# Optimization experiments

Measured on AMD Instinct MI355X. Metric: run time of the kernel, lower is better.

The kernel has to match this reference:

```python
import jax, jax.numpy as jnp
import numpy as np

B, D, E, K = 32768, 512, 64, 4
NCTX = 16
H = (NCTX // 2 - 1) * 768  # 5376: per-expert context block, (n_ctx/2 - 1) rows of ctx_dim=768
NOISE_EPS = 1e-2
LOSS_COEF = 1e-2


def setup_inputs() -> dict:
    key = jax.random.key(0)
    ks = jax.random.split(key, 5)
    x = jax.random.normal(ks[0], (B, D), jnp.float32)
    w_gate = jax.random.normal(ks[1], (D, E), jnp.float32) * 0.02
    w_noise = jax.random.normal(ks[2], (D, E), jnp.float32) * 0.02
    noise = jax.random.normal(ks[3], (B, E), jnp.float32)
    ctx_c = jax.random.normal(ks[4], (E, H), jnp.float32) * 0.02
    return {"x": x, "w_gate": w_gate, "w_noise": w_noise, "noise": noise, "ctx_c": ctx_c}


def _cv_squared(v, eps=1e-10):
    # coefficient-of-variation squared: var / mean^2
    return jnp.var(v) / (jnp.mean(v) ** 2 + eps)


def _normal_cdf(z):
    return 0.5 * (1.0 + jax.lax.erf(z * (1.0 / np.sqrt(2.0))))


def reference(x, w_gate, w_noise, noise, ctx_c):
    # ---- noisy top-k gating (Shazeer sparsely-gated MoE) ----
    clean_logits = x @ w_gate                                    # [B, E]
    noise_stddev = jax.nn.softplus(x @ w_noise) + NOISE_EPS      # [B, E]
    noisy_logits = clean_logits + noise * noise_stddev           # [B, E]

    top_logits, top_idx = jax.lax.top_k(noisy_logits, K + 1)     # [B, K+1]
    top_k_logits = top_logits[:, :K]
    top_k_idx = top_idx[:, :K]
    top_k_gates = jax.nn.softmax(top_k_logits, axis=-1)          # [B, K]

    rows = jnp.arange(B)[:, None]
    gates = jnp.zeros((B, E), x.dtype).at[rows, top_k_idx].set(top_k_gates)  # sparse -> dense scatter

    # ---- load-balancing aux loss ----
    importance = gates.sum(axis=0)                               # [E]
    thr_in = top_logits[:, K][:, None]                           # (K+1)-th largest noisy logit
    thr_out = top_logits[:, K - 1][:, None]                      # K-th largest noisy logit
    is_in = noisy_logits > thr_in
    prob_in = _normal_cdf((clean_logits - thr_in) / noise_stddev)
    prob_out = _normal_cdf((clean_logits - thr_out) / noise_stddev)
    load = jnp.where(is_in, prob_in, prob_out).sum(axis=0)       # [E]
    aux_loss = (_cv_squared(importance) + _cv_squared(load)) * LOSS_COEF

    # ---- weighted combine of per-expert context vectors (as in LPromptLearner) ----
    out = jnp.einsum('be,eh->bh', gates, ctx_c)                  # [B, H]
    return out, aux_loss
```

## Files before the change

### kernel.cpp

```cpp
#include <hip/hip_runtime.h>
#include <math.h>

#define B_ 32768
#define D_ 512
#define E_ 64
#define H_ 5376
#define H4_ (H_ / 4)
#define HC_ 128
#define NCH_ (H_ / HC_)

typedef float f32x4 __attribute__((ext_vector_type(4)));
typedef _Float16 f16x8 __attribute__((ext_vector_type(8)));

__device__ __forceinline__ unsigned short f16bits(_Float16 h) {
    union { _Float16 h; unsigned short u; } c; c.h = h; return c.u;
}

__global__ __launch_bounds__(256) void prep_kernel(
    const float* __restrict__ wgate, const float* __restrict__ wnoise,
    _Float16* __restrict__ wt0, _Float16* __restrict__ wt1)
{
    int e = blockIdx.x;
    int n  = e >> 4, le = e & 15;
    const float* src = (e < E_) ? (wgate + e) : (wnoise + (e - E_));
    for (int k = threadIdx.x; k < D_; k += 256) {
        float v = src[(size_t)k * E_] * 1024.0f;
        _Float16 h0 = (_Float16)v;
        _Float16 h1 = (_Float16)(v - (float)h0);
        int ks = k >> 5, g = (k & 31) >> 3, j = k & 7;
        size_t idx = ((size_t)(ks * 8 + n) * 64 + g * 16 + le) * 8 + j;
        wt0[idx] = h0;
        wt1[idx] = h1;
    }
}

#define TOP5_STEP(TV, TI)                                              \
    {                                                                  \
        double bm = v0; int bj = 0;                                    \
        if (v1 > bm) { bm = v1; bj = 1; }                              \
        if (v2 > bm) { bm = v2; bj = 2; }                              \
        if (v3 > bm) { bm = v3; bj = 3; }                              \
        int be = bj * 16 + le;                                         \
        _Pragma("unroll")                                              \
        for (int off = 1; off < 16; off <<= 1) {                       \
            double om = __shfl_xor(bm, off, 64);                       \
            int    oe = __shfl_xor(be, off, 64);                       \
            if (om > bm || (om == bm && oe < be)) { bm = om; be = oe; }\
        }                                                              \
        TV = bm; TI = be;                                              \
        bool wn = ((be & 15) == le); int sl = be >> 4;                 \
        v0 = (wn && sl == 0) ? -1.0e300 : v0;                          \
        v1 = (wn && sl == 1) ? -1.0e300 : v1;                          \
        v2 = (wn && sl == 2) ? -1.0e300 : v2;                          \
        v3 = (wn && sl == 3) ? -1.0e300 : v3;                          \
    }

__global__ __launch_bounds__(256) void gate_kernel(
    const float* __restrict__ x,
    const _Float16* __restrict__ wt0,
    const _Float16* __restrict__ wt1,
    const float* __restrict__ noise,
    unsigned int* __restrict__ o_idx,
    float4* __restrict__ o_g,
    float* __restrict__ g_imp,
    float* __restrict__ g_load)
{
    __shared__ float s_imp[E_];
    __shared__ float s_load[E_];

    const int t  = threadIdx.x;
    const int w  = t >> 6;
    const int l  = t & 63;
    const int le = l & 15;
    const int g  = l >> 4;
    const int b0 = blockIdx.x * 64;

    if (t < E_) { s_imp[t] = 0.0f; s_load[t] = 0.0f; }
    __syncthreads();

    f32x4 accAC[8], accB[8];
#pragma unroll
    for (int n = 0; n < 8; ++n) {
        accAC[n] = (f32x4){0.f, 0.f, 0.f, 0.f};
        accB[n]  = (f32x4){0.f, 0.f, 0.f, 0.f};
    }

    const float* abase = x + (size_t)(b0 + w * 16 + le) * D_ + g * 8;

#pragma unroll 4
    for (int ks = 0; ks < 16; ++ks) {
        float4 va = *(const float4*)(abase + ks * 32);
        float4 vb = *(const float4*)(abase + ks * 32 + 4);
        float vv[8] = {va.x, va.y, va.z, va.w, vb.x, vb.y, vb.z, vb.w};
        f16x8 a0, a1;
#pragma unroll
        for (int j = 0; j < 8; ++j) {
            float vs = vv[j] * 16.0f;
            _Float16 h = (_Float16)vs;
            a0[j] = h;
            a1[j] = (_Float16)((vs - (float)h) * 4096.0f);
        }
#pragma unroll
        for (int n = 0; n < 8; ++n) {
            size_t boff = ((size_t)(ks * 8 + n) * 64 + l) * 8;
            f16x8 b0f = *(const f16x8*)(wt0 + boff);
            f16x8 b1f = *(const f16x8*)(wt1 + boff);
            accAC[n] = __builtin_amdgcn_mfma_f32_16x16x32_f16(a0, b0f, accAC[n], 0, 0, 0);
            accAC[n] = __builtin_amdgcn_mfma_f32_16x16x32_f16(a0, b1f, accAC[n], 0, 0, 0);
            accB[n]  = __builtin_amdgcn_mfma_f32_16x16x32_f16(a1, b0f, accB[n],  0, 0, 0);
        }
    }

    const double UNSCALE = 1.0 / 16384.0;
    const double RESC    = 1.0 / 4096.0;
    float loadacc[4] = {0.f, 0.f, 0.f, 0.f};
#pragma unroll
    for (int r = 0; r < 4; ++r) {
        int li = w * 16 + g * 4 + r;
        int b  = b0 + li;
        double cl[4], ny[4];
        float  sdf[4];
#pragma unroll
        for (int n = 0; n < 4; ++n) {
            cl[n] = ((double)accAC[n][r] + (double)accB[n][r] * RESC) * UNSCALE;
            float z = (float)(((double)accAC[n+4][r] + (double)accB[n+4][r] * RESC) * UNSCALE);
            float sp = (z > 20.0f) ? z : log1pf(expf(z));
            sdf[n] = sp + 0.01f;
            float nz = noise[(size_t)b * E_ + le + 16 * n];
            ny[n] = cl[n] + (double)(nz * sdf[n]);
        }
        double v0 = ny[0], v1 = ny[1], v2 = ny[2], v3 = ny[3];
        double tv0, tv1, tv2, tv3, tv4;
        int    ti0, ti1, ti2, ti3, ti4;
        TOP5_STEP(tv0, ti0)
        TOP5_STEP(tv1, ti1)
        TOP5_STEP(tv2, ti2)
        TOP5_STEP(tv3, ti3)
        TOP5_STEP(tv4, ti4)
        float e1 = expf((float)(tv1 - tv0)),
              e2 = expf((float)(tv2 - tv0)),
              e3 = expf((float)(tv3 - tv0));
        float inv = 1.0f / (1.0f + e1 + e2 + e3);
        float g0 = inv, g1 = e1 * inv, g2 = e2 * inv, g3 = e3 * inv;
        if (le == 0) {
            o_idx[b] = (unsigned)ti0 | ((unsigned)ti1 << 8) |
                       ((unsigned)ti2 << 16) | ((unsigned)ti3 << 24);
            float4 gv; gv.x = g0; gv.y = g1; gv.z = g2; gv.w = g3;
            o_g[b] = gv;
            atomicAdd(&s_imp[ti0], g0);
            atomicAdd(&s_imp[ti1], g1);
            atomicAdd(&s_imp[ti2], g2);
            atomicAdd(&s_imp[ti3], g3);
        }
        double thr_out = tv3;
        double thr_in  = tv4;
#pragma unroll
        for (int n = 0; n < 4; ++n) {
            double thr = (ny[n] > thr_in) ? thr_in : thr_out;
            float  zz  = (float)(cl[n] - thr) / sdf[n];
            loadacc[n] += 0.5f * (1.0f + erff(zz * 0.70710678118654752f));
        }
    }
#pragma unroll
    for (int n = 0; n < 4; ++n) atomicAdd(&s_load[16 * n + le], loadacc[n]);
    __syncthreads();
    if (t < E_) {
        atomicAdd(&g_imp[t],  s_imp[t]);
        atomicAdd(&g_load[t], s_load[t]);
    }
}

__global__ __launch_bounds__(256) void dispatch_kernel(
    const float* __restrict__ ctx,
    const unsigned int* __restrict__ o_idx,
    const float4* __restrict__ o_g,
    float* __restrict__ out)
{
    __shared__ f32x4 cs[E_ * (HC_ / 4)];

    const int t  = threadIdx.x;
    const int h0 = blockIdx.x * HC_;
    const int tb = blockIdx.y * 64;

#pragma unroll
    for (int i = 0; i < 8; ++i) {
        int idx = t + 256 * i;
        int e = idx >> 5, c = idx & 31;
        cs[idx] = *(const f32x4*)&ctx[(size_t)e * H_ + h0 + c * 4];
    }
    __syncthreads();

    const int tok = t >> 5;
    const int c   = t & 31;
#pragma unroll
    for (int s = 0; s < 8; ++s) {
        int b = tb + s * 8 + tok;
        unsigned pk = o_idx[b];
        float4 g = o_g[b];
        f32x4 r = g.x * cs[((pk      ) & 255u) * 32 + c]
                + g.y * cs[((pk >>  8) & 255u) * 32 + c]
                + g.z * cs[((pk >> 16) & 255u) * 32 + c]
                + g.w * cs[( pk >> 24         ) * 32 + c];
        __builtin_nontemporal_store(r, (f32x4*)&out[(size_t)b * H_ + h0 + c * 4]);
    }
}

__global__ void loss_kernel(const float* __restrict__ g_imp,
                            const float* __restrict__ g_load,
                            float* __restrict__ out)
{
    int e = threadIdx.x;
    double vi = (double)g_imp[e];
    double vl = (double)g_load[e];
    double si = vi, sl = vl;
#pragma unroll
    for (int off = 1; off < 64; off <<= 1) {
        si += __shfl_xor(si, off, 64);
        sl += __shfl_xor(sl, off, 64);
    }
    double mi = si / 64.0, ml = sl / 64.0;
    double di = vi - mi, dl = vl - ml;
    double qi = di * di, ql = dl * dl;
#pragma unroll
    for (int off = 1; off < 64; off <<= 1) {
        qi += __shfl_xor(qi, off, 64);
        ql += __shfl_xor(ql, off, 64);
    }
    double vari = qi / 64.0, varl = ql / 64.0;
    double cv2i = vari / (mi * mi + 1e-10);
    double cv2l = varl / (ml * ml + 1e-10);
    if (e == 0) out[(size_t)B_ * H_] = (float)((cv2i + cv2l) * 0.01);
}

extern "C" void kernel_launch(void* const* d_in, const int* in_sizes, int n_in,
                              void* d_out, int out_size, void* d_ws, size_t ws_size,
                              hipStream_t stream)
{
    const float* x      = (const float*)d_in[0];
    const float* wgate  = (const float*)d_in[1];
    const float* wnoise = (const float*)d_in[2];
    const float* noise  = (const float*)d_in[3];
    const float* ctx    = (const float*)d_in[4];
    float* out    = (float*)d_out;
    float* g_imp  = (float*)d_ws;
    float* g_load = g_imp + E_;
    _Float16* wt0 = (_Float16*)(g_load + E_);
    _Float16* wt1 = wt0 + 128 * D_;
    unsigned int* o_idx = (unsigned int*)(wt1 + 128 * D_);
    float4* o_g = (float4*)(o_idx + B_);

    (void)hipMemsetAsync(d_ws, 0, 2 * E_ * sizeof(float), stream);
    prep_kernel<<<128, 256, 0, stream>>>(wgate, wnoise, wt0, wt1);
    gate_kernel<<<B_ / 64, 256, 0, stream>>>(x, wt0, wt1, noise,
                                             o_idx, o_g, g_imp, g_load);
    dispatch_kernel<<<dim3(NCH_, B_ / 64), 256, 0, stream>>>(ctx, o_idx, o_g, out);
    loss_kernel<<<1, 64, 0, stream>>>(g_imp, g_load, out);
}
```

Before: 199.0 us.

## Stage high-half gate weights in LDS and give each wave 32 rows

The gating GEMM now processes 128 rows per block, with each wave handling two 16-row M tiles that share each loaded B fragment. The hi-part fp16 weights (wt0) are staged into 64KB of shared memory in two K halves, while the lo part is still read from global memory. This cuts global and L2 weight traffic per row and reuses B fragments across two MFMA tiles. In exchange it doubles the accumulator registers, uses a large LDS footprint that may reduce occupancy, and halves the number of blocks to 256.

```diff
diff --git a/kernel.cpp b/kernel.cpp
--- a/kernel.cpp
+++ b/kernel.cpp
@@ -11,6 +11,7 @@
 
 typedef float f32x4 __attribute__((ext_vector_type(4)));
 typedef _Float16 f16x8 __attribute__((ext_vector_type(8)));
+typedef unsigned int u32x4 __attribute__((ext_vector_type(4)));
 
 __device__ __forceinline__ unsigned short f16bits(_Float16 h) {
     union { _Float16 h; unsigned short u; } c; c.h = h; return c.u;
@@ -65,6 +66,7 @@
     float* __restrict__ g_imp,
     float* __restrict__ g_load)
 {
+    __shared__ __align__(16) _Float16 w0s[32768];
     __shared__ float s_imp[E_];
     __shared__ float s_load[E_];
 
@@ -73,92 +75,114 @@
     const int l  = t & 63;
     const int le = l & 15;
     const int g  = l >> 4;
-    const int b0 = blockIdx.x * 64;
+    const int b0 = blockIdx.x * 128;
 
     if (t < E_) { s_imp[t] = 0.0f; s_load[t] = 0.0f; }
-    __syncthreads();
-
-    f32x4 accAC[8], accB[8];
-#pragma unroll
-    for (int n = 0; n < 8; ++n) {
-        accAC[n] = (f32x4){0.f, 0.f, 0.f, 0.f};
-        accB[n]  = (f32x4){0.f, 0.f, 0.f, 0.f};
-    }
-
-    const float* abase = x + (size_t)(b0 + w * 16 + le) * D_ + g * 8;
-
-#pragma unroll 4
-    for (int ks = 0; ks < 16; ++ks) {
-        float4 va = *(const float4*)(abase + ks * 32);
-        float4 vb = *(const float4*)(abase + ks * 32 + 4);
-        float vv[8] = {va.x, va.y, va.z, va.w, vb.x, vb.y, vb.z, vb.w};
-        f16x8 a0, a1;
-#pragma unroll
-        for (int j = 0; j < 8; ++j) {
-            float vs = vv[j] * 16.0f;
-            _Float16 h = (_Float16)vs;
-            a0[j] = h;
-            a1[j] = (_Float16)((vs - (float)h) * 4096.0f);
+
+    f32x4 accAC[2][8], accB[2][8];
+#pragma unroll
+    for (int m = 0; m < 2; ++m)
+#pragma unroll
+        for (int n = 0; n < 8; ++n) {
+            accAC[m][n] = (f32x4){0.f, 0.f, 0.f, 0.f};
+            accB[m][n]  = (f32x4){0.f, 0.f, 0.f, 0.f};
         }
-#pragma unroll
-        for (int n = 0; n < 8; ++n) {
-            size_t boff = ((size_t)(ks * 8 + n) * 64 + l) * 8;
-            f16x8 b0f = *(const f16x8*)(wt0 + boff);
-            f16x8 b1f = *(const f16x8*)(wt1 + boff);
-            accAC[n] = __builtin_amdgcn_mfma_f32_16x16x32_f16(a0, b0f, accAC[n], 0, 0, 0);
-            accAC[n] = __builtin_amdgcn_mfma_f32_16x16x32_f16(a0, b1f, accAC[n], 0, 0, 0);
-            accB[n]  = __builtin_amdgcn_mfma_f32_16x16x32_f16(a1, b0f, accB[n],  0, 0, 0);
+
+    const float* abase0 = x + (size_t)(b0 + w * 32 + le) * D_ + g * 8;
+    const float* abase1 = abase0 + 16 * D_;
+
+#pragma unroll 1
+    for (int kh = 0; kh < 2; ++kh) {
+        __syncthreads();
+        const u32x4* wsrc = (const u32x4*)(wt0 + kh * 32768);
+        u32x4* wdst = (u32x4*)w0s;
+#pragma unroll
+        for (int i = 0; i < 16; ++i) wdst[t + 256 * i] = wsrc[t + 256 * i];
+        __syncthreads();
+
+#pragma unroll 2
+        for (int ks8 = 0; ks8 < 8; ++ks8) {
+            int ks = kh * 8 + ks8;
+            f16x8 a0[2], a1[2];
+#pragma unroll
+            for (int m = 0; m < 2; ++m) {
+                const float* ab = m ? abase1 : abase0;
+                float4 va = *(const float4*)(ab + ks * 32);
+                float4 vb = *(const float4*)(ab + ks * 32 + 4);
+                float vv[8] = {va.x, va.y, va.z, va.w, vb.x, vb.y, vb.z, vb.w};
+#pragma unroll
+                for (int j = 0; j < 8; ++j) {
+                    float vs = vv[j] * 16.0f;
+                    _Float16 h = (_Float16)vs;
+                    a0[m][j] = h;
+                    a1[m][j] = (_Float16)((vs - (float)h) * 4096.0f);
+                }
+            }
+#pragma unroll
+            for (int n = 0; n < 8; ++n) {
+                f16x8 b0f = *(const f16x8*)(w0s + ((size_t)(ks8 * 8 + n) * 64 + l) * 8);
+                f16x8 b1f = *(const f16x8*)(wt1 + ((size_t)(ks * 8 + n) * 64 + l) * 8);
+#pragma unroll
+                for (int m = 0; m < 2; ++m) {
+                    accAC[m][n] = __builtin_amdgcn_mfma_f32_16x16x32_f16(a0[m], b0f, accAC[m][n], 0, 0, 0);
+                    accAC[m][n] = __builtin_amdgcn_mfma_f32_16x16x32_f16(a0[m], b1f, accAC[m][n], 0, 0, 0);
+                    accB[m][n]  = __builtin_amdgcn_mfma_f32_16x16x32_f16(a1[m], b0f, accB[m][n],  0, 0, 0);
+                }
+            }
         }
     }
 
     const double UNSCALE = 1.0 / 16384.0;
     const double RESC    = 1.0 / 4096.0;
     float loadacc[4] = {0.f, 0.f, 0.f, 0.f};
-#pragma unroll
-    for (int r = 0; r < 4; ++r) {
-        int li = w * 16 + g * 4 + r;
-        int b  = b0 + li;
-        double cl[4], ny[4];
-        float  sdf[4];
-#pragma unroll
-        for (int n = 0; n < 4; ++n) {
-            cl[n] = ((double)accAC[n][r] + (double)accB[n][r] * RESC) * UNSCALE;
-            float z = (float)(((double)accAC[n+4][r] + (double)accB[n+4][r] * RESC) * UNSCALE);
-            float sp = (z > 20.0f) ? z : log1pf(expf(z));
-            sdf[n] = sp + 0.01f;
-            float nz = noise[(size_t)b * E_ + le + 16 * n];
-            ny[n] = cl[n] + (double)(nz * sdf[n]);
-        }
-        double v0 = ny[0], v1 = ny[1], v2 = ny[2], v3 = ny[3];
-        double tv0, tv1, tv2, tv3, tv4;
-        int    ti0, ti1, ti2, ti3, ti4;
-        TOP5_STEP(tv0, ti0)
-        TOP5_STEP(tv1, ti1)
-        TOP5_STEP(tv2, ti2)
-        TOP5_STEP(tv3, ti3)
-        TOP5_STEP(tv4, ti4)
-        float e1 = expf((float)(tv1 - tv0)),
-              e2 = expf((float)(tv2 - tv0)),
-              e3 = expf((float)(tv3 - tv0));
-        float inv = 1.0f / (1.0f + e1 + e2 + e3);
-        float g0 = inv, g1 = e1 * inv, g2 = e2 * inv, g3 = e3 * inv;
-        if (le == 0) {
-            o_idx[b] = (unsigned)ti0 | ((unsigned)ti1 << 8) |
-                       ((unsigned)ti2 << 16) | ((unsigned)ti3 << 24);
-            float4 gv; gv.x = g0; gv.y = g1; gv.z = g2; gv.w = g3;
-            o_g[b] = gv;
-            atomicAdd(&s_imp[ti0], g0);
-            atomicAdd(&s_imp[ti1], g1);
-            atomicAdd(&s_imp[ti2], g2);
-            atomicAdd(&s_imp[ti3], g3);
-        }
-        double thr_out = tv3;
-        double thr_in  = tv4;
-#pragma unroll
-        for (int n = 0; n < 4; ++n) {
-            double thr = (ny[n] > thr_in) ? thr_in : thr_out;
-            float  zz  = (float)(cl[n] - thr) / sdf[n];
-            loadacc[n] += 0.5f * (1.0f + erff(zz * 0.70710678118654752f));
+#pragma unroll 1
+    for (int m = 0; m < 2; ++m) {
+#pragma unroll
+        for (int r = 0; r < 4; ++r) {
+            int li = w * 32 + m * 16 + g * 4 + r;
+            int b  = b0 + li;
+            double cl[4], ny[4];
+            float  sdf[4];
+#pragma unroll
+            for (int n = 0; n < 4; ++n) {
+                cl[n] = ((double)accAC[m][n][r] + (double)accB[m][n][r] * RESC) * UNSCALE;
+                float z = (float)(((double)accAC[m][n+4][r] + (double)accB[m][n+4][r] * RESC) * UNSCALE);
+                float sp = (z > 20.0f) ? z : log1pf(expf(z));
+                sdf[n] = sp + 0.01f;
+                float nz = noise[(size_t)b * E_ + le + 16 * n];
+                ny[n] = cl[n] + (double)(nz * sdf[n]);
+            }
+            double v0 = ny[0], v1 = ny[1], v2 = ny[2], v3 = ny[3];
+            double tv0, tv1, tv2, tv3, tv4;
+            int    ti0, ti1, ti2, ti3, ti4;
+            TOP5_STEP(tv0, ti0)
+            TOP5_STEP(tv1, ti1)
+            TOP5_STEP(tv2, ti2)
+            TOP5_STEP(tv3, ti3)
+            TOP5_STEP(tv4, ti4)
+            float e1 = expf((float)(tv1 - tv0)),
+                  e2 = expf((float)(tv2 - tv0)),
+                  e3 = expf((float)(tv3 - tv0));
+            float inv = 1.0f / (1.0f + e1 + e2 + e3);
+            float g0 = inv, g1 = e1 * inv, g2 = e2 * inv, g3 = e3 * inv;
+            if (le == 0) {
+                o_idx[b] = (unsigned)ti0 | ((unsigned)ti1 << 8) |
+                           ((unsigned)ti2 << 16) | ((unsigned)ti3 << 24);
+                float4 gv; gv.x = g0; gv.y = g1; gv.z = g2; gv.w = g3;
+                o_g[b] = gv;
+                atomicAdd(&s_imp[ti0], g0);
+                atomicAdd(&s_imp[ti1], g1);
+                atomicAdd(&s_imp[ti2], g2);
+                atomicAdd(&s_imp[ti3], g3);
+            }
+            double thr_out = tv3;
+            double thr_in  = tv4;
+#pragma unroll
+            for (int n = 0; n < 4; ++n) {
+                double thr = (ny[n] > thr_in) ? thr_in : thr_out;
+                float  zz  = (float)(cl[n] - thr) / sdf[n];
+                loadacc[n] += 0.5f * (1.0f + erff(zz * 0.70710678118654752f));
+            }
         }
     }
 #pragma unroll
@@ -251,8 +275,8 @@
 
     (void)hipMemsetAsync(d_ws, 0, 2 * E_ * sizeof(float), stream);
     prep_kernel<<<128, 256, 0, stream>>>(wgate, wnoise, wt0, wt1);
-    gate_kernel<<<B_ / 64, 256, 0, stream>>>(x, wt0, wt1, noise,
-                                             o_idx, o_g, g_imp, g_load);
+    gate_kernel<<<B_ / 128, 256, 0, stream>>>(x, wt0, wt1, noise,
+                                              o_idx, o_g, g_imp, g_load);
     dispatch_kernel<<<dim3(NCH_, B_ / 64), 256, 0, stream>>>(ctx, o_idx, o_g, out);
     loss_kernel<<<1, 64, 0, stream>>>(g_imp, g_load, out);
 }
```

After: 227.2 us. 14.2% more time.

## Fuse gating and dispatch into one persistent kernel with per-tile ready flags

Applied to the files above, without the earlier changes.

Merges the gate and dispatch kernels into one persistent launch of 1024 blocks. The first 256 blocks compute gating for two token groups each and publish a release flag per group. All blocks then take dispatch tasks (expert-context chunk × token group) and spin on the acquire flag before combining. The goal is to overlap the gating compute with the memory-bound output writes and to drop a kernel boundary. In exchange it adds spin-wait overhead and relies on all blocks being co-resident to avoid deadlock, and the dispatch work is split statically between producer and consumer blocks.

```diff
diff --git a/kernel.cpp b/kernel.cpp
--- a/kernel.cpp
+++ b/kernel.cpp
@@ -8,6 +8,13 @@
 #define H4_ (H_ / 4)
 #define HC_ 128
 #define NCH_ (H_ / HC_)
+#define NTG_ 512
+#define NPROD_ 256
+#define NBLK_ 1024
+#define NCONS_ (NBLK_ - NPROD_)
+#define NTASK_ (NCH_ * NTG_)
+#define CTASK_ 26
+#define PTASK_ 6
 
 typedef float f32x4 __attribute__((ext_vector_type(4)));
 typedef _Float16 f16x8 __attribute__((ext_vector_type(8)));
@@ -55,153 +62,174 @@
         v3 = (wn && sl == 3) ? -1.0e300 : v3;                          \
     }
 
-__global__ __launch_bounds__(256) void gate_kernel(
+__device__ __forceinline__ int rank2tg(int r) {
+    return (r < 256) ? (2 * r) : (2 * (r - 256) + 1);
+}
+
+__global__ __launch_bounds__(256) void moe_kernel(
     const float* __restrict__ x,
     const _Float16* __restrict__ wt0,
     const _Float16* __restrict__ wt1,
     const float* __restrict__ noise,
+    const float* __restrict__ ctx,
+    float* __restrict__ out,
+    float* __restrict__ g_imp,
+    float* __restrict__ g_load,
+    unsigned int* __restrict__ flags,
     unsigned int* __restrict__ o_idx,
-    float4* __restrict__ o_g,
-    float* __restrict__ g_imp,
-    float* __restrict__ g_load)
-{
+    float4* __restrict__ o_g)
+{
+    __shared__ f32x4 cs[E_ * (HC_ / 4)];
     __shared__ float s_imp[E_];
     __shared__ float s_load[E_];
 
+    const int bid = blockIdx.x;
     const int t  = threadIdx.x;
     const int w  = t >> 6;
     const int l  = t & 63;
     const int le = l & 15;
     const int g  = l >> 4;
-    const int b0 = blockIdx.x * 64;
-
-    if (t < E_) { s_imp[t] = 0.0f; s_load[t] = 0.0f; }
-    __syncthreads();
-
-    f32x4 accAC[8], accB[8];
-#pragma unroll
-    for (int n = 0; n < 8; ++n) {
-        accAC[n] = (f32x4){0.f, 0.f, 0.f, 0.f};
-        accB[n]  = (f32x4){0.f, 0.f, 0.f, 0.f};
-    }
-
-    const float* abase = x + (size_t)(b0 + w * 16 + le) * D_ + g * 8;
-
+
+    if (bid < NPROD_) {
+#pragma unroll 1
+        for (int half = 0; half < 2; ++half) {
+            const int tg = 2 * bid + half;
+            const int b0 = tg * 64;
+
+            if (t < E_) { s_imp[t] = 0.0f; s_load[t] = 0.0f; }
+            __syncthreads();
+
+            f32x4 accAC[8], accB[8];
+#pragma unroll
+            for (int n = 0; n < 8; ++n) {
+                accAC[n] = (f32x4){0.f, 0.f, 0.f, 0.f};
+                accB[n]  = (f32x4){0.f, 0.f, 0.f, 0.f};
+            }
+            const float* abase = x + (size_t)(b0 + w * 16 + le) * D_ + g * 8;
 #pragma unroll 4
-    for (int ks = 0; ks < 16; ++ks) {
-        float4 va = *(const float4*)(abase + ks * 32);
-        float4 vb = *(const float4*)(abase + ks * 32 + 4);
-        float vv[8] = {va.x, va.y, va.z, va.w, vb.x, vb.y, vb.z, vb.w};
-        f16x8 a0, a1;
-#pragma unroll
-        for (int j = 0; j < 8; ++j) {
-            float vs = vv[j] * 16.0f;
-            _Float16 h = (_Float16)vs;
-            a0[j] = h;
-            a1[j] = (_Float16)((vs - (float)h) * 4096.0f);
-        }
-#pragma unroll
-        for (int n = 0; n < 8; ++n) {
-            size_t boff = ((size_t)(ks * 8 + n) * 64 + l) * 8;
-            f16x8 b0f = *(const f16x8*)(wt0 + boff);
-            f16x8 b1f = *(const f16x8*)(wt1 + boff);
-            accAC[n] = __builtin_amdgcn_mfma_f32_16x16x32_f16(a0, b0f, accAC[n], 0, 0, 0);
-            accAC[n] = __builtin_amdgcn_mfma_f32_16x16x32_f16(a0, b1f, accAC[n], 0, 0, 0);
-            accB[n]  = __builtin_amdgcn_mfma_f32_16x16x32_f16(a1, b0f, accB[n],  0, 0, 0);
-        }
-    }
-
-    const double UNSCALE = 1.0 / 16384.0;
-    const double RESC    = 1.0 / 4096.0;
-    float loadacc[4] = {0.f, 0.f, 0.f, 0.f};
-#pragma unroll
-    for (int r = 0; r < 4; ++r) {
-        int li = w * 16 + g * 4 + r;
-        int b  = b0 + li;
-        double cl[4], ny[4];
-        float  sdf[4];
-#pragma unroll
-        for (int n = 0; n < 4; ++n) {
-            cl[n] = ((double)accAC[n][r] + (double)accB[n][r] * RESC) * UNSCALE;
-            float z = (float)(((double)accAC[n+4][r] + (double)accB[n+4][r] * RESC) * UNSCALE);
-            float sp = (z > 20.0f) ? z : log1pf(expf(z));
-            sdf[n] = sp + 0.01f;
-            float nz = noise[(size_t)b * E_ + le + 16 * n];
-            ny[n] = cl[n] + (double)(nz * sdf[n]);
-        }
-        double v0 = ny[0], v1 = ny[1], v2 = ny[2], v3 = ny[3];
-        double tv0, tv1, tv2, tv3, tv4;
-        int    ti0, ti1, ti2, ti3, ti4;
-        TOP5_STEP(tv0, ti0)
-        TOP5_STEP(tv1, ti1)
-        TOP5_STEP(tv2, ti2)
-        TOP5_STEP(tv3, ti3)
-        TOP5_STEP(tv4, ti4)
-        float e1 = expf((float)(tv1 - tv0)),
-              e2 = expf((float)(tv2 - tv0)),
-              e3 = expf((float)(tv3 - tv0));
-        float inv = 1.0f / (1.0f + e1 + e2 + e3);
-        float g0 = inv, g1 = e1 * inv, g2 = e2 * inv, g3 = e3 * inv;
-        if (le == 0) {
-            o_idx[b] = (unsigned)ti0 | ((unsigned)ti1 << 8) |
-                       ((unsigned)ti2 << 16) | ((unsigned)ti3 << 24);
-            float4 gv; gv.x = g0; gv.y = g1; gv.z = g2; gv.w = g3;
-            o_g[b] = gv;
-            atomicAdd(&s_imp[ti0], g0);
-            atomicAdd(&s_imp[ti1], g1);
-            atomicAdd(&s_imp[ti2], g2);
-            atomicAdd(&s_imp[ti3], g3);
-        }
-        double thr_out = tv3;
-        double thr_in  = tv4;
-#pragma unroll
-        for (int n = 0; n < 4; ++n) {
-            double thr = (ny[n] > thr_in) ? thr_in : thr_out;
-            float  zz  = (float)(cl[n] - thr) / sdf[n];
-            loadacc[n] += 0.5f * (1.0f + erff(zz * 0.70710678118654752f));
-        }
-    }
-#pragma unroll
-    for (int n = 0; n < 4; ++n) atomicAdd(&s_load[16 * n + le], loadacc[n]);
-    __syncthreads();
-    if (t < E_) {
-        atomicAdd(&g_imp[t],  s_imp[t]);
-        atomicAdd(&g_load[t], s_load[t]);
-    }
-}
-
-__global__ __launch_bounds__(256) void dispatch_kernel(
-    const float* __restrict__ ctx,
-    const unsigned int* __restrict__ o_idx,
-    const float4* __restrict__ o_g,
-    float* __restrict__ out)
-{
-    __shared__ f32x4 cs[E_ * (HC_ / 4)];
-
-    const int t  = threadIdx.x;
-    const int h0 = blockIdx.x * HC_;
-    const int tb = blockIdx.y * 64;
-
-#pragma unroll
-    for (int i = 0; i < 8; ++i) {
-        int idx = t + 256 * i;
-        int e = idx >> 5, c = idx & 31;
-        cs[idx] = *(const f32x4*)&ctx[(size_t)e * H_ + h0 + c * 4];
-    }
-    __syncthreads();
-
-    const int tok = t >> 5;
-    const int c   = t & 31;
-#pragma unroll
-    for (int s = 0; s < 8; ++s) {
-        int b = tb + s * 8 + tok;
-        unsigned pk = o_idx[b];
-        float4 g = o_g[b];
-        f32x4 r = g.x * cs[((pk      ) & 255u) * 32 + c]
-                + g.y * cs[((pk >>  8) & 255u) * 32 + c]
-                + g.z * cs[((pk >> 16) & 255u) * 32 + c]
-                + g.w * cs[( pk >> 24         ) * 32 + c];
-        __builtin_nontemporal_store(r, (f32x4*)&out[(size_t)b * H_ + h0 + c * 4]);
+            for (int ks = 0; ks < 16; ++ks) {
+                float4 va = *(const float4*)(abase + ks * 32);
+                float4 vb = *(const float4*)(abase + ks * 32 + 4);
+                float vv[8] = {va.x, va.y, va.z, va.w, vb.x, vb.y, vb.z, vb.w};
+                f16x8 a0, a1;
+#pragma unroll
+                for (int j = 0; j < 8; ++j) {
+                    float vs = vv[j] * 16.0f;
+                    _Float16 h = (_Float16)vs;
+                    a0[j] = h;
+                    a1[j] = (_Float16)((vs - (float)h) * 4096.0f);
+                }
+#pragma unroll
+                for (int n = 0; n < 8; ++n) {
+                    size_t boff = ((size_t)(ks * 8 + n) * 64 + l) * 8;
+                    f16x8 b0f = *(const f16x8*)(wt0 + boff);
+                    f16x8 b1f = *(const f16x8*)(wt1 + boff);
+                    accAC[n] = __builtin_amdgcn_mfma_f32_16x16x32_f16(a0, b0f, accAC[n], 0, 0, 0);
+                    accAC[n] = __builtin_amdgcn_mfma_f32_16x16x32_f16(a0, b1f, accAC[n], 0, 0, 0);
+                    accB[n]  = __builtin_amdgcn_mfma_f32_16x16x32_f16(a1, b0f, accB[n],  0, 0, 0);
+                }
+            }
+
+            const double UNSCALE = 1.0 / 16384.0;
+            const double RESC    = 1.0 / 4096.0;
+            float loadacc[4] = {0.f, 0.f, 0.f, 0.f};
+#pragma unroll
+            for (int r = 0; r < 4; ++r) {
+                int li = w * 16 + g * 4 + r;
+                int b  = b0 + li;
+                double cl[4], ny[4];
+                float  sdf[4];
+#pragma unroll
+                for (int n = 0; n < 4; ++n) {
+                    cl[n] = ((double)accAC[n][r] + (double)accB[n][r] * RESC) * UNSCALE;
+                    float z = (float)(((double)accAC[n+4][r] + (double)accB[n+4][r] * RESC) * UNSCALE);
+                    float sp = (z > 20.0f) ? z : log1pf(expf(z));
+                    sdf[n] = sp + 0.01f;
+                    float nz = noise[(size_t)b * E_ + le + 16 * n];
+                    ny[n] = cl[n] + (double)(nz * sdf[n]);
+                }
+                double v0 = ny[0], v1 = ny[1], v2 = ny[2], v3 = ny[3];
+                double tv0, tv1, tv2, tv3, tv4;
+                int    ti0, ti1, ti2, ti3, ti4;
+                TOP5_STEP(tv0, ti0)
+                TOP5_STEP(tv1, ti1)
+                TOP5_STEP(tv2, ti2)
+                TOP5_STEP(tv3, ti3)
+                TOP5_STEP(tv4, ti4)
+                float e1 = expf((float)(tv1 - tv0)),
+                      e2 = expf((float)(tv2 - tv0)),
+                      e3 = expf((float)(tv3 - tv0));
+                float inv = 1.0f / (1.0f + e1 + e2 + e3);
+                float g0 = inv, g1 = e1 * inv, g2 = e2 * inv, g3 = e3 * inv;
+                if (le == 0) {
+                    o_idx[b] = (unsigned)ti0 | ((unsigned)ti1 << 8) |
+                               ((unsigned)ti2 << 16) | ((unsigned)ti3 << 24);
+                    float4 gv; gv.x = g0; gv.y = g1; gv.z = g2; gv.w = g3;
+                    o_g[b] = gv;
+                    atomicAdd(&s_imp[ti0], g0);
+                    atomicAdd(&s_imp[ti1], g1);
+                    atomicAdd(&s_imp[ti2], g2);
+                    atomicAdd(&s_imp[ti3], g3);
+                }
+                double thr_out = tv3;
+                double thr_in  = tv4;
+#pragma unroll
+                for (int n = 0; n < 4; ++n) {
+                    double thr = (ny[n] > thr_in) ? thr_in : thr_out;
+                    float  zz  = (float)(cl[n] - thr) / sdf[n];
+                    loadacc[n] += 0.5f * (1.0f + erff(zz * 0.70710678118654752f));
+                }
+            }
+#pragma unroll
+            for (int n = 0; n < 4; ++n) atomicAdd(&s_load[16 * n + le], loadacc[n]);
+            __syncthreads();
+            if (t == 0)
+                __hip_atomic_store(&flags[tg], 1u, __ATOMIC_RELEASE,
+                                   __HIP_MEMORY_SCOPE_AGENT);
+            if (t < E_) {
+                atomicAdd(&g_imp[t],  s_imp[t]);
+                atomicAdd(&g_load[t], s_load[t]);
+            }
+        }
+    }
+
+    const int ntask = (bid < NPROD_) ? PTASK_ : CTASK_;
+#pragma unroll 1
+    for (int k = 0; k < ntask; ++k) {
+        int j = (bid < NPROD_) ? (CTASK_ * NCONS_ + bid + NPROD_ * k)
+                               : ((bid - NPROD_) + NCONS_ * k);
+        int r  = j & (NTG_ - 1);
+        int ch = j >> 9;
+        int tg = rank2tg(r);
+        int h0 = ch * HC_;
+
+        __syncthreads();
+#pragma unroll
+        for (int i = 0; i < 8; ++i) {
+            int idx = t + 256 * i;
+            int e = idx >> 5, c2 = idx & 31;
+            cs[idx] = *(const f32x4*)&ctx[(size_t)e * H_ + h0 + c2 * 4];
+        }
+        if (t == 0) {
+            while (__hip_atomic_load(&flags[tg], __ATOMIC_ACQUIRE,
+                                     __HIP_MEMORY_SCOPE_AGENT) == 0)
+                __builtin_amdgcn_s_sleep(16);
+        }
+        __syncthreads();
+
+        const int tok = t >> 5;
+        const int c2  = t & 31;
+#pragma unroll
+        for (int s = 0; s < 8; ++s) {
+            int b = tg * 64 + s * 8 + tok;
+            unsigned pk = o_idx[b];
+            float4 gv = o_g[b];
+            f32x4 rr = gv.x * cs[((pk      ) & 255u) * 32 + c2]
+                     + gv.y * cs[((pk >>  8) & 255u) * 32 + c2]
+                     + gv.z * cs[((pk >> 16) & 255u) * 32 + c2]
+                     + gv.w * cs[( pk >> 24         ) * 32 + c2];
+            __builtin_nontemporal_store(rr, (f32x4*)&out[(size_t)b * H_ + h0 + c2 * 4]);
+        }
     }
 }
 
@@ -244,15 +272,15 @@
     float* out    = (float*)d_out;
     float* g_imp  = (float*)d_ws;
     float* g_load = g_imp + E_;
-    _Float16* wt0 = (_Float16*)(g_load + E_);
+    unsigned int* flags = (unsigned int*)(g_load + E_);
+    _Float16* wt0 = (_Float16*)(flags + NTG_);
     _Float16* wt1 = wt0 + 128 * D_;
     unsigned int* o_idx = (unsigned int*)(wt1 + 128 * D_);
     float4* o_g = (float4*)(o_idx + B_);
 
-    (void)hipMemsetAsync(d_ws, 0, 2 * E_ * sizeof(float), stream);
+    (void)hipMemsetAsync(d_ws, 0, (2 * E_ + NTG_) * sizeof(unsigned int), stream);
     prep_kernel<<<128, 256, 0, stream>>>(wgate, wnoise, wt0, wt1);
-    gate_kernel<<<B_ / 64, 256, 0, stream>>>(x, wt0, wt1, noise,
-                                             o_idx, o_g, g_imp, g_load);
-    dispatch_kernel<<<dim3(NCH_, B_ / 64), 256, 0, stream>>>(ctx, o_idx, o_g, out);
+    moe_kernel<<<NBLK_, 256, 0, stream>>>(x, wt0, wt1, noise, ctx, out,
+                                          g_imp, g_load, flags, o_idx, o_g);
     loss_kernel<<<1, 64, 0, stream>>>(g_imp, g_load, out);
 }
```

Result: slower. 729.7 us (+266.7%).
